# Kernel tuning notes

Measured on AMD Instinct MI355X. Metric: run time of the kernel, lower is better.

The kernel has to match this reference:

```python
import jax, jax.numpy as jnp
import numpy as np

B, T, D_MODEL, D_K = 4, 4096, 1024, 64

def setup_inputs() -> dict:
    key = jax.random.key(0)
    k1, k2, k3, k4, k5 = jax.random.split(key, 5)
    x = jax.random.normal(k1, (B, T, D_MODEL), dtype=jnp.float32)
    # rotary freqs_cis as (real, imag) pairs: unit-magnitude like real RoPE
    theta = 10000.0
    inv = 1.0 / (theta ** (jnp.arange(0, D_K, 2, dtype=jnp.float32) / D_K))  # [D_K//2]
    ang = jnp.arange(T, dtype=jnp.float32)[:, None] * inv[None, :]           # [T, D_K//2]
    freqs_cis = jnp.stack([jnp.cos(ang), jnp.sin(ang)], axis=-1)             # [T, D_K//2, 2]
    scale = 1.0 / np.sqrt(D_MODEL)
    Wq = jax.random.normal(k2, (D_MODEL, D_K), dtype=jnp.float32) * scale
    Wk = jax.random.normal(k3, (D_MODEL, D_K), dtype=jnp.float32) * scale
    Wv = jax.random.normal(k4, (D_MODEL, D_K), dtype=jnp.float32) * scale
    return {"x": x, "freqs_cis": freqs_cis, "Wq": Wq, "Wk": Wk, "Wv": Wv}

def _apply_rope(t, fr, fi):
    # t: [B,T,D_K]; fr/fi: [T, D_K//2]. Complex mult on (even, odd) pairs.
    tp = t.reshape(*t.shape[:-1], D_K // 2, 2)       # [B,T,P,2]
    tr, ti = tp[..., 0], tp[..., 1]
    or_ = tr * fr - ti * fi
    oi_ = tr * fi + ti * fr
    return jnp.stack([or_, oi_], axis=-1).reshape(*t.shape[:-1], D_K)

def reference(x, freqs_cis, Wq, Wk, Wv):
    q = x @ Wq                                       # [B,T,D_K]
    k = x @ Wk
    v = x @ Wv
    fr, fi = freqs_cis[..., 0], freqs_cis[..., 1]    # [T, D_K//2]
    q = _apply_rope(q, fr, fi)
    k = _apply_rope(k, fr, fi)
    wei = jnp.einsum('btd,bsd->bts', q, k) * (D_K ** -0.5)   # [B,T,T]
    causal = jnp.tril(jnp.ones((T, T), dtype=bool))
    wei = jnp.where(causal, wei, -jnp.inf)
    wei = jax.nn.softmax(wei, axis=-1)
    return jnp.einsum('bts,bsd->btd', wei, v)        # [B,T,D_K]
```

## Files before the change

### kernel.cpp

```cpp
#include <hip/hip_runtime.h>
#include <hip/hip_bf16.h>

#define BB 4
#define TT 4096
#define DM 1024
#define DK 64
#define NSPLIT 8

using f32x4  = __attribute__((ext_vector_type(4))) float;
using bf16x8 = __attribute__((ext_vector_type(8))) short;

__device__ __forceinline__ short f2bf(float f) {
    __hip_bfloat16 h = __float2bfloat16(f);
    return __builtin_bit_cast(short, h);
}
__device__ __forceinline__ float bf2f(short s) {
    unsigned int u = ((unsigned int)(unsigned short)s) << 16;
    return __builtin_bit_cast(float, u);
}

__global__ __launch_bounds__(256) void wt_kernel(const float* __restrict__ Wq,
                                                 const float* __restrict__ Wk,
                                                 const float* __restrict__ Wv,
                                                 short* __restrict__ Wt) {
    int idx = blockIdx.x * 256 + threadIdx.x;
    if (idx >= 192 * 1024) return;
    int n = idx >> 10;
    int m = idx & 1023;
    const float* W = (n < 64) ? Wq : (n < 128) ? Wk : Wv;
    int c = n & 63;
    Wt[idx] = f2bf(W[m * 64 + c]);
}

__global__ __launch_bounds__(256, 3) void proj_rope(const float* __restrict__ x,
                                                    const float* __restrict__ freqs,
                                                    const short* __restrict__ Wt,
                                                    short* __restrict__ q,
                                                    short* __restrict__ k,
                                                    short* __restrict__ vt)
{
    __shared__ float As[2][4096];
    __shared__ short Bs[2][4096];

    int t  = threadIdx.x;
    int w  = t >> 6;
    int l  = t & 63;
    int lr = l & 15;
    int lg = (l >> 4) & 3;
    int bx = blockIdx.x;
    int mt = (bx & 7) * 32 + (bx >> 3) / 3;
    int nh = (bx >> 3) % 3;
    int m0 = mt * 64;

    int arow = t >> 2, au = (t & 3) * 4;
    int brow = t >> 2, bu = (t & 3) * 2;
    const float* gA = x  + (size_t)(m0 + arow) * DM + au * 4;
    const short* gB = Wt + (size_t)(nh * 64 + brow) * DM + bu * 8;
    int aswz = arow & 7, bswz = brow & 7;

    f32x4 ar[4]; bf16x8 br[2];

#define LOADG(c_) do { int kk = (c_) << 6;                     \
        ar[0] = *(const f32x4*)(gA + kk);                      \
        ar[1] = *(const f32x4*)(gA + kk + 4);                  \
        ar[2] = *(const f32x4*)(gA + kk + 8);                  \
        ar[3] = *(const f32x4*)(gA + kk + 12);                 \
        br[0] = *(const bf16x8*)(gB + kk);                     \
        br[1] = *(const bf16x8*)(gB + kk + 8);                 \
    } while (0)

#define WRITELDS(buf_) do {                                                    \
        int sa = arow * 64;                                                    \
        *(f32x4*)&As[buf_][sa + (((au + 0) ^ aswz) << 2)] = ar[0];             \
        *(f32x4*)&As[buf_][sa + (((au + 1) ^ aswz) << 2)] = ar[1];             \
        *(f32x4*)&As[buf_][sa + (((au + 2) ^ aswz) << 2)] = ar[2];             \
        *(f32x4*)&As[buf_][sa + (((au + 3) ^ aswz) << 2)] = ar[3];             \
        int sb = brow * 64;                                                    \
        *(bf16x8*)&Bs[buf_][sb + (((bu + 0) ^ bswz) << 3)] = br[0];            \
        *(bf16x8*)&Bs[buf_][sb + (((bu + 1) ^ bswz) << 3)] = br[1];            \
    } while (0)

    f32x4 acc[4];
#pragma unroll
    for (int i = 0; i < 4; ++i) acc[i] = (f32x4){0.f, 0.f, 0.f, 0.f};

    LOADG(0); WRITELDS(0); LOADG(1);
    __syncthreads();

    int cur = 0;
    int r7 = lr & 7;
    int amrow = (w * 16 + lr) * 64;
    for (int ch = 0; ch < 16; ++ch) {
#pragma unroll
        for (int s = 0; s < 2; ++s) {
            int u0 = s * 8 + lg * 2;
            f32x4 a0 = *(const f32x4*)&As[cur][amrow + (((u0    ) ^ r7) << 2)];
            f32x4 a1 = *(const f32x4*)&As[cur][amrow + (((u0 + 1) ^ r7) << 2)];
            bf16x8 af;
#pragma unroll
            for (int j = 0; j < 4; ++j) { af[j] = f2bf(a0[j]); af[4 + j] = f2bf(a1[j]); }
            int ub = s * 4 + lg;
#pragma unroll
            for (int nt = 0; nt < 4; ++nt) {
                bf16x8 bfr = *(const bf16x8*)&Bs[cur][(nt * 16 + lr) * 64 + ((ub ^ r7) << 3)];
                acc[nt] = __builtin_amdgcn_mfma_f32_16x16x32_bf16(af, bfr, acc[nt], 0, 0, 0);
            }
        }
        if (ch + 1 < 16) {
            WRITELDS(cur ^ 1);
            if (ch + 2 < 16) LOADG(ch + 2);
            __syncthreads();
            cur ^= 1;
        }
    }
#undef LOADG
#undef WRITELDS

    __syncthreads();

    if (nh == 2) {
        short* vs = &Bs[0][0];
#pragma unroll
        for (int r = 0; r < 4; ++r)
#pragma unroll
            for (int nt = 0; nt < 4; ++nt)
                vs[(w * 16 + lg * 4 + r) * 64 + nt * 16 + lr] = f2bf(acc[nt][r]);
        __syncthreads();
        int b   = mt >> 6;
        int tt0 = (mt & 63) * 64;
        int c   = t >> 2;
        int toff = (t & 3) * 16;
        bf16x8 v0, v1;
#pragma unroll
        for (int j = 0; j < 8; ++j) {
            v0[j] = vs[(toff + j) * 64 + c];
            v1[j] = vs[(toff + 8 + j) * 64 + c];
        }
        short* dstv = vt + ((size_t)b * DK + c) * TT + tt0 + toff;
        *(bf16x8*)dstv = v0;
        *(bf16x8*)(dstv + 8) = v1;
    } else {
        short* dst = nh ? k : q;
        float postscale = nh ? 1.0f : 0.125f;
#pragma unroll
        for (int r = 0; r < 4; ++r) {
            int tg = m0 + w * 16 + lg * 4 + r;
            int tt = tg & (TT - 1);
#pragma unroll
            for (int nt = 0; nt < 4; ++nt) {
                int c = nt * 16 + lr;
                float e = acc[nt][r];
                float p = __shfl_xor(e, 1);
                float2 f = ((const float2*)freqs)[(size_t)tt * 32 + (c >> 1)];
                float sgn = (c & 1) ? f.y : -f.y;
                dst[(size_t)tg * DK + c] = f2bf((e * f.x + p * sgn) * postscale);
            }
        }
    }
}

__global__ __launch_bounds__(256, 4) void attn_kernel(const short* __restrict__ q,
                                                      const short* __restrict__ k,
                                                      const short* __restrict__ vt,
                                                      short* __restrict__ po,
                                                      float* __restrict__ ml)
{
    __shared__ short Kb[64][64];
    __shared__ short Vb[64][64];
    __shared__ short pbuf[4][16][72];

    int w  = threadIdx.x >> 6;
    int l  = threadIdx.x & 63;
    int lr = l & 15;
    int lg = l >> 4;
    int b  = blockIdx.y;
    int s  = blockIdx.z;
    int qt = 63 - blockIdx.x;
    int q0 = qt * 64;
    int qrow_wave = q0 + w * 16;

    const short* qB = q  + (size_t)b * TT * DK;
    const short* kB = k  + (size_t)b * TT * DK;
    const short* vB = vt + (size_t)b * DK * TT;

    bf16x8 qf0 = *(const bf16x8*)(qB + (size_t)(qrow_wave + lr) * DK + 8 * lg);
    bf16x8 qf1 = *(const bf16x8*)(qB + (size_t)(qrow_wave + lr) * DK + 32 + 8 * lg);

    f32x4 of[4];
#pragma unroll
    for (int i = 0; i < 4; ++i) of[i] = (f32x4){0.f, 0.f, 0.f, 0.f};
    float m[4], lsum[4];
#pragma unroll
    for (int r = 0; r < 4; ++r) { m[r] = -INFINITY; lsum[r] = 0.f; }

    int nt = (qt >= s) ? ((qt - s + NSPLIT) >> 3) : 0;

    int srow = threadIdx.x >> 2;
    int u0   = (threadIdx.x & 3) * 2;
    int p0s  = ((u0) ^ (srow & 7)) * 8;
    int p1s  = ((u0 + 1) ^ (srow & 7)) * 8;

    bf16x8 kr0, kr1, vr0, vr1;
    short* mypb = &pbuf[w][0][0];

#define ISSUE(tile_) do {                                                        \
        int kv0_ = (tile_) << 6;                                                 \
        const short* gk_ = kB + (size_t)(kv0_ + srow) * DK + (u0 * 8);           \
        const short* gv_ = vB + (size_t)srow * TT + kv0_ + (u0 * 8);             \
        kr0 = *(const bf16x8*)gk_; kr1 = *(const bf16x8*)(gk_ + 8);              \
        vr0 = *(const bf16x8*)gv_; vr1 = *(const bf16x8*)(gv_ + 8);              \
    } while (0)

#define WRITE() do {                                                             \
        *(bf16x8*)&Kb[srow][p0s] = kr0;                                         \
        *(bf16x8*)&Kb[srow][p1s] = kr1;                                         \
        *(bf16x8*)&Vb[srow][p0s] = vr0;                                         \
        *(bf16x8*)&Vb[srow][p1s] = vr1;                                         \
    } while (0)

    if (nt > 0) {
        ISSUE(s); WRITE();
        if (nt > 1) ISSUE(s + NSPLIT);
        __syncthreads();
        for (int i = 0; i < nt; ++i) {
            int kv0 = (s + i * NSPLIT) << 6;

            f32x4 sc[4];
#pragma unroll
            for (int c = 0; c < 4; ++c) sc[c] = (f32x4){0.f, 0.f, 0.f, 0.f};
#pragma unroll
            for (int c = 0; c < 4; ++c) {
                int row = c * 16 + lr;
                bf16x8 kf0 = *(const bf16x8*)&Kb[row][((lg) ^ (row & 7)) * 8];
                bf16x8 kf1 = *(const bf16x8*)&Kb[row][((4 + lg) ^ (row & 7)) * 8];
                sc[c] = __builtin_amdgcn_mfma_f32_16x16x32_bf16(qf0, kf0, sc[c], 0, 0, 0);
                sc[c] = __builtin_amdgcn_mfma_f32_16x16x32_bf16(qf1, kf1, sc[c], 0, 0, 0);
            }

            if (kv0 == q0) {
#pragma unroll
                for (int r = 0; r < 4; ++r) {
                    int qg = qrow_wave + lg * 4 + r;
#pragma unroll
                    for (int c = 0; c < 4; ++c)
                        sc[c][r] = (kv0 + c * 16 + lr <= qg) ? sc[c][r] : -INFINITY;
                }
            }

            float mx[4];
#pragma unroll
            for (int r = 0; r < 4; ++r)
                mx[r] = fmaxf(fmaxf(sc[0][r], sc[1][r]), fmaxf(sc[2][r], sc[3][r]));
            bool needA = (mx[0] > m[0] + 8.f) || (mx[1] > m[1] + 8.f) ||
                         (mx[2] > m[2] + 8.f) || (mx[3] > m[3] + 8.f);
            if (__any(needA)) {
#pragma unroll
                for (int r = 0; r < 4; ++r) {
                    float t2 = mx[r];
                    t2 = fmaxf(t2, __shfl_xor(t2, 1));
                    t2 = fmaxf(t2, __shfl_xor(t2, 2));
                    t2 = fmaxf(t2, __shfl_xor(t2, 4));
                    t2 = fmaxf(t2, __shfl_xor(t2, 8));
                    float mn = fmaxf(m[r], t2);
                    float alpha = __expf(m[r] - mn);
                    m[r] = mn;
                    lsum[r] *= alpha;
#pragma unroll
                    for (int dt = 0; dt < 4; ++dt) of[dt][r] *= alpha;
                }
            }
#pragma unroll
            for (int r = 0; r < 4; ++r) {
                float p0 = __expf(sc[0][r] - m[r]);
                float p1 = __expf(sc[1][r] - m[r]);
                float p2 = __expf(sc[2][r] - m[r]);
                float p3 = __expf(sc[3][r] - m[r]);
                float ps = (p0 + p1) + (p2 + p3);
                ps += __shfl_xor(ps, 1);
                ps += __shfl_xor(ps, 2);
                ps += __shfl_xor(ps, 4);
                ps += __shfl_xor(ps, 8);
                lsum[r] += ps;
                int prow = (lg * 4 + r) * 72;
                mypb[prow + lr]      = f2bf(p0);
                mypb[prow + 16 + lr] = f2bf(p1);
                mypb[prow + 32 + lr] = f2bf(p2);
                mypb[prow + 48 + lr] = f2bf(p3);
            }

#pragma unroll
            for (int ks = 0; ks < 2; ++ks) {
                bf16x8 pa = *(const bf16x8*)(mypb + lr * 72 + ks * 32 + 8 * lg);
#pragma unroll
                for (int dt = 0; dt < 4; ++dt) {
                    int row = dt * 16 + lr;
                    bf16x8 vf = *(const bf16x8*)&Vb[row][((ks * 4 + lg) ^ (row & 7)) * 8];
                    of[dt] = __builtin_amdgcn_mfma_f32_16x16x32_bf16(pa, vf, of[dt], 0, 0, 0);
                }
            }

            if (i + 1 < nt) {
                __syncthreads();
                WRITE();
                if (i + 2 < nt) ISSUE(s + (i + 2) * NSPLIT);
                __syncthreads();
            }
        }
    }
#undef ISSUE
#undef WRITE

    short* myo  = po + (((size_t)b * 64 + qt) * NSPLIT + s) * 4096;
    float* myml = ml + (((size_t)b * 64 + qt) * NSPLIT + s) * 128;
#pragma unroll
    for (int r = 0; r < 4; ++r) {
        int row = w * 16 + lg * 4 + r;
#pragma unroll
        for (int dt = 0; dt < 4; ++dt) myo[row * 64 + dt * 16 + lr] = f2bf(of[dt][r]);
        if (lr == 0) { myml[row] = m[r]; myml[64 + row] = lsum[r]; }
    }
}

__global__ __launch_bounds__(256) void merge_kernel(const short* __restrict__ po,
                                                    const float* __restrict__ ml,
                                                    float* __restrict__ out)
{
    int qt = blockIdx.x;
    int b  = blockIdx.y;
    int row = threadIdx.x >> 2;
    int cg  = threadIdx.x & 3;

    size_t mlbase = ((size_t)b * 64 + qt) * NSPLIT * 128;
    float mm[NSPLIT], llv[NSPLIT];
#pragma unroll
    for (int s = 0; s < NSPLIT; ++s) {
        mm[s]  = ml[mlbase + s * 128 + row];
        llv[s] = ml[mlbase + s * 128 + 64 + row];
    }
    float M = -INFINITY;
#pragma unroll
    for (int s = 0; s < NSPLIT; ++s) M = fmaxf(M, mm[s]);
    float e[NSPLIT], den = 0.f;
#pragma unroll
    for (int s = 0; s < NSPLIT; ++s) { e[s] = __expf(mm[s] - M); den += e[s] * llv[s]; }
    float inv = 1.0f / den;

    size_t pbase = ((size_t)b * 64 + qt) * NSPLIT * 4096;
#pragma unroll
    for (int j = 0; j < 2; ++j) {
        int col = cg * 16 + j * 8;
        float acc8[8];
#pragma unroll
        for (int e2 = 0; e2 < 8; ++e2) acc8[e2] = 0.f;
#pragma unroll
        for (int s = 0; s < NSPLIT; ++s) {
            bf16x8 v = *(const bf16x8*)(po + pbase + s * 4096 + row * 64 + col);
#pragma unroll
            for (int e2 = 0; e2 < 8; ++e2) acc8[e2] += e[s] * bf2f(v[e2]);
        }
        float* orow = out + ((size_t)b * TT + qt * 64 + row) * DK + col;
#pragma unroll
        for (int e2 = 0; e2 < 8; ++e2) orow[e2] = acc8[e2] * inv;
    }
}

extern "C" void kernel_launch(void* const* d_in, const int* in_sizes, int n_in,
                              void* d_out, int out_size, void* d_ws, size_t ws_size,
                              hipStream_t stream) {
    const float* x     = (const float*)d_in[0];
    const float* freqs = (const float*)d_in[1];
    const float* Wq    = (const float*)d_in[2];
    const float* Wk    = (const float*)d_in[3];
    const float* Wv    = (const float*)d_in[4];
    float* out = (float*)d_out;

    char* ws = (char*)d_ws;
    short* Wt  = (short*)ws;
    short* qb  = (short*)(ws + 393216);
    short* kb  = (short*)(ws + 2490368);
    short* vtb = (short*)(ws + 4587520);
    short* po  = (short*)(ws + 6684672);
    float* ml  = (float*)(ws + 23461888);

    hipLaunchKernelGGL(wt_kernel, dim3(768), dim3(256), 0, stream, Wq, Wk, Wv, Wt);
    hipLaunchKernelGGL(proj_rope, dim3(768), dim3(256), 0, stream, x, freqs, Wt, qb, kb, vtb);
    hipLaunchKernelGGL(attn_kernel, dim3(64, BB, NSPLIT), dim3(256), 0, stream, qb, kb, vtb, po, ml);
    hipLaunchKernelGGL(merge_kernel, dim3(64, BB), dim3(256), 0, stream, po, ml, out);
}
```

Baseline: 70.82 us.

## Halve KV tile to 32 rows, skip fully-masked waves, defer row-sum reduction

Shrinks the K/V shared-memory tiles from 64 to 32 keys, changing the swizzles and load mapping, and raises the launch bound to 8 blocks per CU. With finer tiles, waves whose query rows lie entirely before a tile skip its compute, which trims wasted work on the causal diagonal. The per-tile cross-lane sum of softmax probabilities is replaced by per-lane accumulation with one reduction at the end. The trade-off is more iterations and barriers per unit of work, plus smaller MFMA batches per tile.

```diff
diff --git a/kernel.cpp b/kernel.cpp
--- a/kernel.cpp
+++ b/kernel.cpp
@@ -159,15 +159,15 @@
     }
 }
 
-__global__ __launch_bounds__(256, 4) void attn_kernel(const short* __restrict__ q,
+__global__ __launch_bounds__(256, 8) void attn_kernel(const short* __restrict__ q,
                                                       const short* __restrict__ k,
                                                       const short* __restrict__ vt,
                                                       short* __restrict__ po,
                                                       float* __restrict__ ml)
 {
-    __shared__ short Kb[64][64];
-    __shared__ short Vb[64][64];
-    __shared__ short pbuf[4][16][72];
+    __shared__ short Kb[32][64];
+    __shared__ short Vb[64][32];
+    __shared__ short pbuf[4][16][40];
 
     int w  = threadIdx.x >> 6;
     int l  = threadIdx.x & 63;
@@ -193,122 +193,118 @@
 #pragma unroll
     for (int r = 0; r < 4; ++r) { m[r] = -INFINITY; lsum[r] = 0.f; }
 
-    int nt = (qt >= s) ? ((qt - s + NSPLIT) >> 3) : 0;
-
-    int srow = threadIdx.x >> 2;
-    int u0   = (threadIdx.x & 3) * 2;
-    int p0s  = ((u0) ^ (srow & 7)) * 8;
-    int p1s  = ((u0 + 1) ^ (srow & 7)) * 8;
-
-    bf16x8 kr0, kr1, vr0, vr1;
+    int ntot = 2 * qt + 2;
+    int nt   = (s < ntot) ? ((ntot - 1 - s) / NSPLIT + 1) : 0;
+
+    int krow = threadIdx.x >> 3, ku = threadIdx.x & 7;
+    int vrow = threadIdx.x >> 2, vu = threadIdx.x & 3;
+    int kdst = krow * 64 + ((ku ^ (krow & 7)) << 3);
+    int vdst = vrow * 32 + ((vu ^ ((vrow >> 1) & 3)) << 3);
+    const short* gk0 = kB + (size_t)krow * DK + ku * 8;
+    const short* gv0 = vB + (size_t)vrow * TT + vu * 8;
+
+    bf16x8 kr, vr;
     short* mypb = &pbuf[w][0][0];
-
-#define ISSUE(tile_) do {                                                        \
-        int kv0_ = (tile_) << 6;                                                 \
-        const short* gk_ = kB + (size_t)(kv0_ + srow) * DK + (u0 * 8);           \
-        const short* gv_ = vB + (size_t)srow * TT + kv0_ + (u0 * 8);             \
-        kr0 = *(const bf16x8*)gk_; kr1 = *(const bf16x8*)(gk_ + 8);              \
-        vr0 = *(const bf16x8*)gv_; vr1 = *(const bf16x8*)(gv_ + 8);              \
+    short* Kf = &Kb[0][0];
+    short* Vf = &Vb[0][0];
+
+#define ISSUE(tile_) do {                                   \
+        int kv0_ = (tile_) << 5;                            \
+        kr = *(const bf16x8*)(gk0 + (size_t)kv0_ * DK);     \
+        vr = *(const bf16x8*)(gv0 + kv0_);                  \
     } while (0)
 
-#define WRITE() do {                                                             \
-        *(bf16x8*)&Kb[srow][p0s] = kr0;                                         \
-        *(bf16x8*)&Kb[srow][p1s] = kr1;                                         \
-        *(bf16x8*)&Vb[srow][p0s] = vr0;                                         \
-        *(bf16x8*)&Vb[srow][p1s] = vr1;                                         \
+#define WRITE() do {                                        \
+        *(bf16x8*)(Kf + kdst) = kr;                         \
+        *(bf16x8*)(Vf + vdst) = vr;                         \
     } while (0)
 
     if (nt > 0) {
-        ISSUE(s); WRITE();
-        if (nt > 1) ISSUE(s + NSPLIT);
-        __syncthreads();
+        ISSUE(s);
         for (int i = 0; i < nt; ++i) {
-            int kv0 = (s + i * NSPLIT) << 6;
-
-            f32x4 sc[4];
-#pragma unroll
-            for (int c = 0; c < 4; ++c) sc[c] = (f32x4){0.f, 0.f, 0.f, 0.f};
-#pragma unroll
-            for (int c = 0; c < 4; ++c) {
-                int row = c * 16 + lr;
-                bf16x8 kf0 = *(const bf16x8*)&Kb[row][((lg) ^ (row & 7)) * 8];
-                bf16x8 kf1 = *(const bf16x8*)&Kb[row][((4 + lg) ^ (row & 7)) * 8];
-                sc[c] = __builtin_amdgcn_mfma_f32_16x16x32_bf16(qf0, kf0, sc[c], 0, 0, 0);
-                sc[c] = __builtin_amdgcn_mfma_f32_16x16x32_bf16(qf1, kf1, sc[c], 0, 0, 0);
-            }
-
-            if (kv0 == q0) {
+            int tile = s + i * NSPLIT;
+            int kv0  = tile << 5;
+            WRITE();
+            if (i + 1 < nt) ISSUE(tile + NSPLIT);
+            __syncthreads();
+
+            if (kv0 <= qrow_wave) {
+                f32x4 sc[2];
+#pragma unroll
+                for (int c = 0; c < 2; ++c) {
+                    int row = c * 16 + lr;
+                    int swz = row & 7;
+                    sc[c] = (f32x4){0.f, 0.f, 0.f, 0.f};
+                    bf16x8 kf0 = *(const bf16x8*)(Kf + row * 64 + ((lg ^ swz) << 3));
+                    bf16x8 kf1 = *(const bf16x8*)(Kf + row * 64 + (((4 + lg) ^ swz) << 3));
+                    sc[c] = __builtin_amdgcn_mfma_f32_16x16x32_bf16(qf0, kf0, sc[c], 0, 0, 0);
+                    sc[c] = __builtin_amdgcn_mfma_f32_16x16x32_bf16(qf1, kf1, sc[c], 0, 0, 0);
+                }
+
+                if (kv0 + 32 > qrow_wave) {
+#pragma unroll
+                    for (int r = 0; r < 4; ++r) {
+                        int qg = qrow_wave + lg * 4 + r;
+#pragma unroll
+                        for (int c = 0; c < 2; ++c)
+                            sc[c][r] = (kv0 + c * 16 + lr <= qg) ? sc[c][r] : -INFINITY;
+                    }
+                }
+
+                float mx[4];
+#pragma unroll
+                for (int r = 0; r < 4; ++r) mx[r] = fmaxf(sc[0][r], sc[1][r]);
+                bool needA = (mx[0] > m[0] + 8.f) || (mx[1] > m[1] + 8.f) ||
+                             (mx[2] > m[2] + 8.f) || (mx[3] > m[3] + 8.f);
+                if (__any(needA)) {
+#pragma unroll
+                    for (int r = 0; r < 4; ++r) {
+                        float t2 = mx[r];
+                        t2 = fmaxf(t2, __shfl_xor(t2, 1));
+                        t2 = fmaxf(t2, __shfl_xor(t2, 2));
+                        t2 = fmaxf(t2, __shfl_xor(t2, 4));
+                        t2 = fmaxf(t2, __shfl_xor(t2, 8));
+                        float mn = fmaxf(m[r], t2);
+                        float alpha = __expf(m[r] - mn);
+                        m[r] = mn;
+                        lsum[r] *= alpha;
+#pragma unroll
+                        for (int dt = 0; dt < 4; ++dt) of[dt][r] *= alpha;
+                    }
+                }
 #pragma unroll
                 for (int r = 0; r < 4; ++r) {
-                    int qg = qrow_wave + lg * 4 + r;
-#pragma unroll
-                    for (int c = 0; c < 4; ++c)
-                        sc[c][r] = (kv0 + c * 16 + lr <= qg) ? sc[c][r] : -INFINITY;
-                }
-            }
-
-            float mx[4];
-#pragma unroll
-            for (int r = 0; r < 4; ++r)
-                mx[r] = fmaxf(fmaxf(sc[0][r], sc[1][r]), fmaxf(sc[2][r], sc[3][r]));
-            bool needA = (mx[0] > m[0] + 8.f) || (mx[1] > m[1] + 8.f) ||
-                         (mx[2] > m[2] + 8.f) || (mx[3] > m[3] + 8.f);
-            if (__any(needA)) {
-#pragma unroll
-                for (int r = 0; r < 4; ++r) {
-                    float t2 = mx[r];
-                    t2 = fmaxf(t2, __shfl_xor(t2, 1));
-                    t2 = fmaxf(t2, __shfl_xor(t2, 2));
-                    t2 = fmaxf(t2, __shfl_xor(t2, 4));
-                    t2 = fmaxf(t2, __shfl_xor(t2, 8));
-                    float mn = fmaxf(m[r], t2);
-                    float alpha = __expf(m[r] - mn);
-                    m[r] = mn;
-                    lsum[r] *= alpha;
-#pragma unroll
-                    for (int dt = 0; dt < 4; ++dt) of[dt][r] *= alpha;
-                }
-            }
-#pragma unroll
-            for (int r = 0; r < 4; ++r) {
-                float p0 = __expf(sc[0][r] - m[r]);
-                float p1 = __expf(sc[1][r] - m[r]);
-                float p2 = __expf(sc[2][r] - m[r]);
-                float p3 = __expf(sc[3][r] - m[r]);
-                float ps = (p0 + p1) + (p2 + p3);
-                ps += __shfl_xor(ps, 1);
-                ps += __shfl_xor(ps, 2);
-                ps += __shfl_xor(ps, 4);
-                ps += __shfl_xor(ps, 8);
-                lsum[r] += ps;
-                int prow = (lg * 4 + r) * 72;
-                mypb[prow + lr]      = f2bf(p0);
-                mypb[prow + 16 + lr] = f2bf(p1);
-                mypb[prow + 32 + lr] = f2bf(p2);
-                mypb[prow + 48 + lr] = f2bf(p3);
-            }
-
-#pragma unroll
-            for (int ks = 0; ks < 2; ++ks) {
-                bf16x8 pa = *(const bf16x8*)(mypb + lr * 72 + ks * 32 + 8 * lg);
+                    float p0 = __expf(sc[0][r] - m[r]);
+                    float p1 = __expf(sc[1][r] - m[r]);
+                    lsum[r] += p0 + p1;
+                    int prow = (lg * 4 + r) * 40;
+                    mypb[prow + lr]      = f2bf(p0);
+                    mypb[prow + 16 + lr] = f2bf(p1);
+                }
+
+                bf16x8 pa = *(const bf16x8*)(mypb + lr * 40 + 8 * lg);
 #pragma unroll
                 for (int dt = 0; dt < 4; ++dt) {
                     int row = dt * 16 + lr;
-                    bf16x8 vf = *(const bf16x8*)&Vb[row][((ks * 4 + lg) ^ (row & 7)) * 8];
+                    bf16x8 vf = *(const bf16x8*)(Vf + row * 32 + ((lg ^ ((row >> 1) & 3)) << 3));
                     of[dt] = __builtin_amdgcn_mfma_f32_16x16x32_bf16(pa, vf, of[dt], 0, 0, 0);
                 }
             }
-
-            if (i + 1 < nt) {
-                __syncthreads();
-                WRITE();
-                if (i + 2 < nt) ISSUE(s + (i + 2) * NSPLIT);
-                __syncthreads();
-            }
+            if (i + 1 < nt) __syncthreads();
         }
     }
 #undef ISSUE
 #undef WRITE
+
+#pragma unroll
+    for (int r = 0; r < 4; ++r) {
+        float ps = lsum[r];
+        ps += __shfl_xor(ps, 1);
+        ps += __shfl_xor(ps, 2);
+        ps += __shfl_xor(ps, 4);
+        ps += __shfl_xor(ps, 8);
+        lsum[r] = ps;
+    }
 
     short* myo  = po + (((size_t)b * 64 + qt) * NSPLIT + s) * 4096;
     float* myml = ml + (((size_t)b * 64 + qt) * NSPLIT + s) * 128;
```

Result: slower. 86.86 us (+22.6%).
